# Optimization experiments

Measured on AMD Instinct MI355X. Metric: run time of the kernel, lower is better.

Reference implementation:

```python
import jax, jax.numpy as jnp
import numpy as np
import math

D, NS, PP, POS = 256, 4, 4, 16
PI = math.pi
LN_EPS = 1e-5


def _gelu(x):
    return jax.nn.gelu(x, approximate=False)  # torch default GELU is exact erf


def _mlp(x, W1, b1, W2, b2):
    return _gelu(x @ W1 + b1) @ W2 + b2


def setup_inputs() -> dict:
    key = jax.random.key(0)
    ks = jax.random.split(key, 16)

    def lin(k, fi, fo):
        k1, k2 = jax.random.split(k)
        s = 1.0 / np.sqrt(fi)
        W = jax.random.uniform(k1, (fi, fo), minval=-s, maxval=s, dtype=jnp.float32)
        b = jax.random.uniform(k2, (fo,), minval=-s, maxval=s, dtype=jnp.float32)
        return W, b

    x = jax.random.normal(ks[0], (2, 2048, D), dtype=jnp.float32)
    kW1, kb1 = lin(ks[1], D, D); kW2, kb2 = lin(ks[2], D, NS * PP)
    qW1, qb1 = lin(ks[3], D, D); qW2, qb2 = lin(ks[4], D, NS * PP)
    vW, vb = lin(ks[5], D, D)
    oW, ob = lin(ks[6], D, D)
    gW1, gb1 = lin(ks[7], D, D // 2); gW2, gb2 = lin(ks[8], D // 2, 1)
    lW1, lb1 = lin(ks[9], D, D); lW2, lb2 = lin(ks[10], D, POS)
    lvW, lvb = lin(ks[11], D, D)
    pos_freqs = jnp.exp(jnp.arange(POS, dtype=jnp.float32) * (-math.log(10000.0) / POS))
    return dict(
        x=x, kW1=kW1, kb1=kb1, kW2=kW2, kb2=kb2,
        qW1=qW1, qb1=qb1, qW2=qW2, qb2=qb2, vW=vW, vb=vb,
        ln_g=jnp.ones((D,), jnp.float32), ln_b=jnp.zeros((D,), jnp.float32), oW=oW, ob=ob,
        set_weights=jnp.ones((NS,), jnp.float32), pos_freqs=pos_freqs,
        pos_weight=jnp.ones((1,), jnp.float32),
        gW1=gW1, gb1=gb1, gW2=gW2, gb2=gb2,
        lW1=lW1, lb1=lb1, lW2=lW2, lb2=lb2, lvW=lvW, lvb=lvb,
        surprise_scale=jnp.float32(1.0), surprise_bias=jnp.float32(0.0),
        ltm_weight=jnp.float32(0.5),
    )


def _fwd(x, kW1, kb1, kW2, kb2, qW1, qb1, qW2, qb2, vW, vb, ln_g, ln_b, oW, ob,
         set_weights, pos_freqs, pos_weight, gW1, gb1, gW2, gb2,
         lW1, lb1, lW2, lb2, lvW, lvb, surprise_scale, surprise_bias, ltm_weight):
    B, L, Dd = x.shape
    key_phasor = jnp.exp(1j * (jnp.tanh(_mlp(x, kW1, kb1, kW2, kb2)) * PI)).reshape(B, L, NS, PP)
    query_phasor = jnp.exp(1j * (jnp.tanh(_mlp(x, qW1, qb1, qW2, qb2)) * PI)).reshape(B, L, NS, PP)
    V_real = x @ vW + vb  # (B,L,D)
    weights = jax.nn.softmax(set_weights)

    pos_cb = jnp.maximum(jnp.arange(L, dtype=jnp.float32), 1.0)  # shifted positions, clamp(min=1)

    # ---- cross-bank (joint product over sets) + surprise write gate ----
    joint_key = jnp.prod(key_phasor, axis=2)    # (B,L,PP)
    joint_query = jnp.prod(query_phasor, axis=2)
    km_shift = jnp.concatenate(
        [jnp.zeros_like(joint_key[:, :1]), jnp.cumsum(joint_key[:, :-1], axis=1)], axis=1)
    res_mag = jnp.abs((km_shift * jnp.conj(joint_key)).sum(-1))  # (B,L)
    familiarity = jnp.clip(res_mag / (pos_cb * math.sqrt(PP)), 0.0, 1.0)[..., None]
    write_gate = jax.nn.sigmoid(surprise_scale * ((1.0 - familiarity) - 0.5) + surprise_bias)
    V_gated = (V_real * write_gate).astype(jnp.complex64)

    bound = joint_key[..., None] * V_gated[:, :, None, :]       # (B,L,PP,D)
    memory = jnp.cumsum(bound, axis=1)
    cross_bank = (memory * jnp.conj(joint_query)[..., None]).sum(2).real  # (B,L,D)

    # ---- per-bank binding/retrieval ----
    bound_all = key_phasor[..., None] * V_gated[:, :, None, None, :]  # (B,L,NS,PP,D)
    mem_all = jnp.cumsum(bound_all, axis=1)
    retr_per_bank = (mem_all * jnp.conj(query_phasor)[..., None]).sum(3).real  # (B,L,NS,D)
    total = (retr_per_bank * weights[None, None, :, None]).sum(2)
    total = (total + cross_bank) / (NS + 1)

    # ---- positional phasor bank ----
    V = V_real.astype(jnp.complex64)
    pos_phasor = jnp.exp(1j * (jnp.arange(L, dtype=jnp.float32)[:, None] * pos_freqs * 2 * PI))  # (L,POS)
    bound_pos = pos_phasor[None, :, :, None] * V[:, :, None, :]  # (B,L,POS,D)
    mem_pos = jnp.cumsum(bound_pos, axis=1)
    retr_pos = (mem_pos * jnp.conj(pos_phasor)[None, :, :, None]).sum(2).real
    gate = jax.nn.sigmoid(_mlp(x, gW1, gb1, gW2, gb2))  # (B,L,1)
    total = gate * total + (1 - gate) * (jax.nn.sigmoid(pos_weight) * retr_pos)

    # ---- LTM bank with surprise gating ----
    ltm_kp = jnp.exp(1j * (jnp.tanh(_mlp(x, lW1, lb1, lW2, lb2)) * PI))  # (B,L,POS)
    ltm_val = x @ lvW + lvb
    km2 = jnp.concatenate(
        [jnp.zeros_like(ltm_kp[:, :1]), jnp.cumsum(ltm_kp[:, :-1], axis=1)], axis=1)
    res2 = jnp.abs((km2 * jnp.conj(ltm_kp)).sum(-1))
    fam2 = jnp.clip(res2 / (pos_cb * math.sqrt(POS)), 0.0, 1.0)[..., None]
    wg2 = jax.nn.sigmoid(surprise_scale * ((1.0 - fam2) - 0.5) + surprise_bias)  # (B,L,1)
    gated_bind = wg2[:, :, None, :] * ltm_kp[..., None] * ltm_val.astype(jnp.complex64)[:, :, None, :]
    ltm_mem = jnp.cumsum(gated_bind, axis=1)                      # (B,L,POS,D)
    ltm_retr = (ltm_mem * jnp.conj(ltm_kp)[..., None]).sum(2).real
    pos1 = jnp.arange(1, L + 1, dtype=jnp.float32)
    ltm_retr = ltm_retr / jnp.sqrt(pos1 * POS)[None, :, None]
    total = total + jax.nn.sigmoid(ltm_weight) * ltm_retr

    # ---- output projection: LayerNorm + Linear, residual ----
    t = total / jnp.sqrt(pos1 * PP)[None, :, None]
    mu = t.mean(-1, keepdims=True)
    var = t.var(-1, keepdims=True)
    tn = (t - mu) / jnp.sqrt(var + LN_EPS) * ln_g + ln_b
    return x + tn @ oW + ob


def reference(x, kW1, kb1, kW2, kb2, qW1, qb1, qW2, qb2, vW, vb, ln_g, ln_b, oW, ob,
              set_weights, pos_freqs, pos_weight, gW1, gb1, gW2, gb2,
              lW1, lb1, lW2, lb2, lvW, lvb, surprise_scale, surprise_bias, ltm_weight):
    return _fwd(x, kW1, kb1, kW2, kb2, qW1, qb1, qW2, qb2, vW, vb, ln_g, ln_b, oW, ob,
                set_weights, pos_freqs, pos_weight, gW1, gb1, gW2, gb2,
                lW1, lb1, lW2, lb2, lvW, lvb, surprise_scale, surprise_bias, ltm_weight)
```

## Files before the change

kernel.cpp:

```cpp
#include <hip/hip_runtime.h>
#include <math.h>

#define DD   256
#define NSB  4
#define PPB  4
#define POSB 16
#define LL   2048
#define BB   2
#define NC   64
#define CHK  32
#define NG   13
#define FS   128
#define PI_F 3.14159265358979323846f

#define JK_OFF   0
#define JQ_OFF   8
#define KP_OFF   16
#define QP_OFF   48
#define LKP_OFF  80
#define GATE_OFF 112

#define FEAT_O  0L
#define V_O     524288L
#define LV_O    1572864L
#define PPH_O   2621440L
#define TOT_O   2686976L
#define CMEM_O  3735552L
#define WGB_O   7143424L
#define TOT2_O  7151616L
#define WS_FLOATS 8200192L
#define KM_O    CMEM_O
#define XH_O    CMEM_O
#define XL_O    (CMEM_O + 524288L)
#define WTH_O   (CMEM_O + 1048576L)
#define WT2H_O  (CMEM_O + 1245184L)

typedef __attribute__((ext_vector_type(8))) short bf16x8;
typedef __attribute__((ext_vector_type(4))) float f32x4;

__device__ __forceinline__ float sigm(float v){ return 1.0f/(1.0f+expf(-v)); }
__device__ __forceinline__ float gelu_exact(float v){ return 0.5f*v*(1.0f+erff(v*0.70710678118654752f)); }
__device__ __forceinline__ unsigned short f2bf(float f){
    unsigned u = __float_as_uint(f);
    unsigned r = u + 0x7fffu + ((u>>16)&1u);
    return (unsigned short)(r>>16);
}
__device__ __forceinline__ float bf2f(unsigned short h){ return __uint_as_float(((unsigned)h)<<16); }

__global__ __launch_bounds__(256) void prep_all(
    const float* __restrict__ x,
    const float* __restrict__ kW1, const float* __restrict__ qW1, const float* __restrict__ lW1,
    const float* __restrict__ vW,  const float* __restrict__ lvW, const float* __restrict__ gW1,
    const float* __restrict__ kW2, const float* __restrict__ qW2, const float* __restrict__ lW2,
    const float* __restrict__ pf,
    unsigned short* __restrict__ xh, unsigned short* __restrict__ xl,
    unsigned short* __restrict__ wth, unsigned short* __restrict__ wt2h,
    float* __restrict__ posph)
{
    int bid = blockIdx.x, tid = threadIdx.x;
    if (bid < 512){
        int gid = bid*256 + tid;
        int frag = gid>>6, lane = gid&63;
        int tile = frag>>3, ksb = frag&7;
        int row = tile*16 + (lane&15);
        int k0  = ksb*32 + ((lane>>4)&3)*8;
        const float* xp = x + (long)row*DD + k0;
        unsigned short h8[8], l8[8];
        #pragma unroll
        for (int e=0;e<8;++e){
            float f = xp[e];
            unsigned short h = f2bf(f);
            h8[e] = h;
            l8[e] = f2bf(f - bf2f(h));
        }
        *(bf16x8*)(xh + (long)gid*8) = *(bf16x8*)h8;
        *(bf16x8*)(xl + (long)gid*8) = *(bf16x8*)l8;
    } else if (bid < 512+192){
        int gid = (bid-512)*256 + tid;
        int frag = gid>>6, lane = gid&63;
        int tile = frag>>3, ksb = frag&7;
        int col = tile*16 + (lane&15);
        int k0  = ksb*32 + ((lane>>4)&3)*8;
        unsigned short h8[8];
        #pragma unroll
        for (int e=0;e<8;++e){
            int fi = k0 + e;
            float w = 0.f;
            if (col < 1408){
                int m = col >> 8;
                if (m < 5){
                    const float* W = (m==0)?kW1:((m==1)?qW1:((m==2)?lW1:((m==3)?vW:lvW)));
                    w = W[(long)fi*DD + (col & 255)];
                } else {
                    w = gW1[(long)fi*128 + (col - 1280)];
                }
            }
            h8[e] = f2bf(w);
        }
        *(bf16x8*)(wth + (long)gid*8) = *(bf16x8*)h8;
    } else if (bid < 512+192+48){
        int blk = bid - (512+192);
        int m = blk>>4, o = blk&15;
        const float* W2 = (m==0)?kW2:((m==1)?qW2:lW2);
        wt2h[(long)blk*DD + tid] = f2bf(W2[tid*16+o]);
    } else {
        int t = (bid - (512+192+48))*256 + tid;
        if (t < LL){
            #pragma unroll
            for (int j=0;j<POSB;++j){
                float ang = (((float)t * pf[j]) * 2.0f) * PI_F;
                float s,c; sincosf(ang,&s,&c);
                posph[t*32+2*j]   = c;
                posph[t*32+2*j+1] = s;
            }
        }
    }
}

__global__ __launch_bounds__(256) void mlp_fused(
    const unsigned short* __restrict__ xh, const unsigned short* __restrict__ xl,
    const unsigned short* __restrict__ wth, const unsigned short* __restrict__ wt2h,
    const float* __restrict__ kb1, const float* __restrict__ kb2,
    const float* __restrict__ qb1, const float* __restrict__ qb2,
    const float* __restrict__ lb1, const float* __restrict__ lb2,
    const float* __restrict__ vb,  const float* __restrict__ lvb,
    const float* __restrict__ gb1, const float* __restrict__ gW2, const float* __restrict__ gb2,
    float* __restrict__ feat, float* __restrict__ Vbuf, float* __restrict__ lvalbuf)
{
    __shared__ __align__(16) char smraw[18432];
    int tid = threadIdx.x, lane = tid & 63, wv = tid >> 6;
    int mat = blockIdx.x >> 7, bm = blockIdx.x & 127;
    int rowg0 = bm*32;
    int ar = lane & 15, kk = (lane>>4)*8;

    f32x4 acc[2][4];
    #pragma unroll
    for (int i=0;i<2;++i)
        #pragma unroll
        for (int j=0;j<4;++j) acc[i][j] = (f32x4){0.f,0.f,0.f,0.f};

    bf16x8 ah[2], al[2], bh[4];
    {
        #pragma unroll
        for (int i=0;i<2;++i){
            long off = (((long)(2*bm+i)*8 + 0)*64 + lane)*8;
            ah[i] = *reinterpret_cast<const bf16x8*>(xh + off);
            al[i] = *reinterpret_cast<const bf16x8*>(xl + off);
        }
        #pragma unroll
        for (int j=0;j<4;++j){
            long off = (((long)(mat*16 + wv*4 + j)*8 + 0)*64 + lane)*8;
            bh[j] = *reinterpret_cast<const bf16x8*>(wth + off);
        }
    }
    #pragma unroll
    for (int ksb=0; ksb<8; ++ksb){
        bf16x8 nah[2], nal[2], nbh[4];
        if (ksb < 7){
            #pragma unroll
            for (int i=0;i<2;++i){
                long off = (((long)(2*bm+i)*8 + ksb+1)*64 + lane)*8;
                nah[i] = *reinterpret_cast<const bf16x8*>(xh + off);
                nal[i] = *reinterpret_cast<const bf16x8*>(xl + off);
            }
            #pragma unroll
            for (int j=0;j<4;++j){
                long off = (((long)(mat*16 + wv*4 + j)*8 + ksb+1)*64 + lane)*8;
                nbh[j] = *reinterpret_cast<const bf16x8*>(wth + off);
            }
        }
        #pragma unroll
        for (int i=0;i<2;++i)
            #pragma unroll
            for (int j=0;j<4;++j){
                acc[i][j] = __builtin_amdgcn_mfma_f32_16x16x32_bf16(ah[i], bh[j], acc[i][j], 0,0,0);
                acc[i][j] = __builtin_amdgcn_mfma_f32_16x16x32_bf16(al[i], bh[j], acc[i][j], 0,0,0);
            }
        if (ksb < 7){
            #pragma unroll
            for (int i=0;i<2;++i){ ah[i]=nah[i]; al[i]=nal[i]; }
            #pragma unroll
            for (int j=0;j<4;++j) bh[j]=nbh[j];
        }
    }

    int rl0 = (lane>>4)*4;

    if (mat < 3){
        float (*ang)[16] = (float(*)[16])(smraw + 16384);
        const float* b1 = (mat==0)?kb1:((mat==1)?qb1:lb1);
        #pragma unroll
        for (int i=0;i<2;++i)
            #pragma unroll
            for (int j=0;j<4;++j){
                int c = wv*64 + j*16 + ar;
                #pragma unroll
                for (int r=0;r<4;++r){
                    int row = i*16 + rl0 + r;
                    float hv = gelu_exact(acc[i][j][r] + b1[c]);
                    int bo = row*512 + c*2;
                    *(unsigned short*)(smraw + (bo ^ ((row&7)<<4))) = f2bf(hv);
                }
            }
        __syncthreads();
        const float* b2 = (mat==0)?kb2:((mat==1)?qb2:lb2);
        int off = (mat==0)?KP_OFF:((mat==1)?QP_OFF:LKP_OFF);
        if (wv < 2){
            int arow = wv*16 + ar;
            f32x4 a2 = (f32x4){0.f,0.f,0.f,0.f};
            #pragma unroll
            for (int ksb=0; ksb<8; ++ksb){
                int k = ksb*32 + kk;
                int bo = arow*512 + k*2;
                bf16x8 af = *reinterpret_cast<const bf16x8*>(smraw + (bo ^ ((arow&7)<<4)));
                bf16x8 bf = *reinterpret_cast<const bf16x8*>(wt2h + ((long)(mat*16 + ar)*DD + k));
                a2 = __builtin_amdgcn_mfma_f32_16x16x32_bf16(af, bf, a2, 0,0,0);
            }
            int o = ar;
            #pragma unroll
            for (int r=0;r<4;++r){
                int tok = wv*16 + rl0 + r;
                float a = tanhf(a2[r] + b2[o])*PI_F;
                ang[tok][o] = a;
                float sn,cs; sincosf(a,&sn,&cs);
                long rowg = rowg0 + tok;
                feat[rowg*FS + off + 2*o]   = cs;
                feat[rowg*FS + off + 2*o+1] = sn;
            }
        }
        __syncthreads();
        if (mat<2 && tid<128){
            int tok = tid>>2, p = tid&3;
            float a = ang[tok][p]+ang[tok][4+p]+ang[tok][8+p]+ang[tok][12+p];
            float sn,cs; sincosf(a,&sn,&cs);
            int joff = (mat==0)?JK_OFF:JQ_OFF;
            long rowg = rowg0 + tok;
            feat[rowg*FS + joff + 2*p]   = cs;
            feat[rowg*FS + joff + 2*p+1] = sn;
        }
    } else if (mat < 5){
        const float* bv = (mat==3)? vb : lvb;
        float* dst = (mat==3)? Vbuf : lvalbuf;
        #pragma unroll
        for (int i=0;i<2;++i)
            #pragma unroll
            for (int j=0;j<4;++j){
                int c = wv*64 + j*16 + ar;
                #pragma unroll
                for (int r=0;r<4;++r)
                    dst[(long)(rowg0 + i*16 + rl0 + r)*DD + c] = acc[i][j][r] + bv[c];
            }
    } else {
        float (*hg)[132] = (float(*)[132])smraw;
        float (*part)[8] = (float(*)[8])(smraw + 32*132*4);
        if (wv < 2){
            #pragma unroll
            for (int i=0;i<2;++i)
                #pragma unroll
                for (int j=0;j<4;++j){
                    int c = wv*64 + j*16 + ar;
                    #pragma unroll
                    for (int r=0;r<4;++r)
                        hg[i*16 + rl0 + r][c] = gelu_exact(acc[i][j][r] + gb1[c]);
                }
        }
        __syncthreads();
        {
            int tok = tid>>3, jj = tid&7;
            float s = 0.f;
            #pragma unroll
            for (int c=0;c<16;++c) s += hg[tok][jj*16+c]*gW2[jj*16+c];
            part[tok][jj] = s;
        }
        __syncthreads();
        if (tid < 32){
            float s = gb2[0];
            #pragma unroll
            for (int j=0;j<8;++j) s += part[tid][j];
            feat[(long)(rowg0+tid)*FS + GATE_OFF] = sigm(s);
        }
    }
}

__global__ __launch_bounds__(256) void g_prefix(const float* __restrict__ feat, float* __restrict__ km){
    int b = blockIdx.x / 40, ch = blockIdx.x % 40;
    int off = (ch<8) ? (JK_OFF+ch) : (LKP_OFF + (ch-8));
    int tid = threadIdx.x;
    long rb = (long)b*LL*FS;
    float v[8]; float s = 0.f;
    #pragma unroll
    for (int u=0;u<8;++u){
        v[u] = feat[rb + (long)(tid*8+u)*FS + off];
        s += v[u];
    }
    int lane = tid & 63, w = tid >> 6;
    float xsc = s;
    #pragma unroll
    for (int o=1;o<64;o<<=1){ float y = __shfl_up(xsc,o); if (lane>=o) xsc += y; }
    __shared__ float wsum[4];
    if (lane==63) wsum[w] = xsc;
    __syncthreads();
    float woff = 0.f;
    for (int i=0;i<w;++i) woff += wsum[i];
    float run = (xsc - s) + woff;
    #pragma unroll
    for (int u=0;u<8;++u){
        km[((long)b*LL + tid*8+u)*40 + ch] = run;
        run += v[u];
    }
}

__global__ __launch_bounds__(256) void g_fam(
    const float* __restrict__ feat, const float* __restrict__ km,
    const float* __restrict__ ss_p, const float* __restrict__ sb_p,
    float* __restrict__ wgbuf)
{
    int t = blockIdx.x*256 + threadIdx.x;
    if (t >= BB*LL) return;
    int tc = t % LL;
    float ss = ss_p[0], sb = sb_p[0];
    long frow = (long)t*FS;
    const float* kmrow = km + (long)t*40;
    float pcb = fmaxf((float)tc, 1.0f);

    float sr=0.f, si=0.f;
    #pragma unroll
    for (int p=0;p<4;++p){
        float kr = feat[frow+JK_OFF+2*p], ki = feat[frow+JK_OFF+2*p+1];
        float kmr = kmrow[2*p], kmi = kmrow[2*p+1];
        sr += kmr*kr + kmi*ki;
        si += kmi*kr - kmr*ki;
    }
    float res = sqrtf(sr*sr+si*si);
    float fam = fminf(fmaxf(res/(pcb*2.0f),0.f),1.f);
    wgbuf[(long)t*2] = sigm(ss*(0.5f-fam)+sb);

    sr=0.f; si=0.f;
    #pragma unroll
    for (int p=0;p<16;++p){
        float kr = feat[frow+LKP_OFF+2*p], ki = feat[frow+LKP_OFF+2*p+1];
        float kmr = kmrow[8+2*p], kmi = kmrow[8+2*p+1];
        sr += kmr*kr + kmi*ki;
        si += kmi*kr - kmr*ki;
    }
    float res2 = sqrtf(sr*sr+si*si);
    float fam2 = fminf(fmaxf(res2/(pcb*4.0f),0.f),1.f);
    wgbuf[(long)t*2+1] = sigm(ss*(0.5f-fam2)+sb);
}

__global__ __launch_bounds__(128) void m_chunksum(
    const float* __restrict__ feat, const float* __restrict__ posph,
    const float* __restrict__ wgbuf, const float* __restrict__ Vbuf,
    const float* __restrict__ lvalbuf, float* __restrict__ cmem)
{
    int blk = blockIdx.x;
    int dh = blk & 1; blk >>= 1;
    int b = blk/(NG*NC); int r = blk%(NG*NC); int g = r/NC, c = r%NC;
    int d = dh*128 + threadIdx.x;
    __shared__ __align__(16) float4 kl4[CHK][2];
    __shared__ float gl[CHK];
    long frow = ((long)b*LL + c*CHK)*FS;
    for (int idx=threadIdx.x; idx<CHK*2; idx+=128){
        int t = idx>>1, j = idx&1;
        float4 v;
        if (g==0)       v = *(const float4*)&feat[frow + (long)t*FS + JK_OFF + j*4];
        else if (g<5)   v = *(const float4*)&feat[frow + (long)t*FS + KP_OFF + (g-1)*8 + j*4];
        else if (g<9)   v = *(const float4*)&posph[(long)(c*CHK+t)*32 + (g-5)*8 + j*4];
        else            v = *(const float4*)&feat[frow + (long)t*FS + LKP_OFF + (g-9)*8 + j*4];
        kl4[t][j] = v;
    }
    for (int t=threadIdx.x; t<CHK; t+=128){
        float gf;
        if (g<5)      gf = wgbuf[((long)b*LL + c*CHK + t)*2];
        else if (g<9) gf = 1.0f;
        else          gf = wgbuf[((long)b*LL + c*CHK + t)*2 + 1];
        gl[t] = gf;
    }
    __syncthreads();
    const float* vsrc = (g>=9)? lvalbuf : Vbuf;
    long vrow = ((long)b*LL + c*CHK)*DD + d;
    float m0r=0,m0i=0,m1r=0,m1i=0,m2r=0,m2i=0,m3r=0,m3i=0;
    float vnext = vsrc[vrow];
    #pragma unroll 4
    for (int t=0;t<CHK;++t){
        float v = vnext * gl[t];
        if (t+1 < CHK) vnext = vsrc[vrow + (long)(t+1)*DD];
        float4 ka = kl4[t][0], kb = kl4[t][1];
        m0r += ka.x*v; m0i += ka.y*v;
        m1r += ka.z*v; m1i += ka.w*v;
        m2r += kb.x*v; m2i += kb.y*v;
        m3r += kb.z*v; m3i += kb.w*v;
    }
    long grp = (long)((b*NG+g)*NC + c);
    long ob = grp*8*DD + d;
    cmem[ob+0*DD]=m0r; cmem[ob+1*DD]=m0i;
    cmem[ob+2*DD]=m1r; cmem[ob+3*DD]=m1i;
    cmem[ob+4*DD]=m2r; cmem[ob+5*DD]=m2i;
    cmem[ob+6*DD]=m3r; cmem[ob+7*DD]=m3i;
}

__global__ __launch_bounds__(256) void m_scan(float* __restrict__ cmem){
    int line = blockIdx.x;
    int comp = line & 1; int l2 = line >> 1;
    int lb = l2>>2, slot = l2&3, d = threadIdx.x;
    float v[NC];
    #pragma unroll
    for (int c=0;c<NC;++c){
        long a = ((((long)(lb*NC + c)*4 + slot)*2) + comp)*DD + d;
        v[c] = cmem[a];
    }
    float run = 0.f;
    #pragma unroll
    for (int c=0;c<NC;++c){
        long a = ((((long)(lb*NC + c)*4 + slot)*2) + comp)*DD + d;
        cmem[a] = run;
        run += v[c];
    }
}

__global__ __launch_bounds__(128) void m_retrieve2(
    const float* __restrict__ feat, const float* __restrict__ posph,
    const float* __restrict__ wgbuf, const float* __restrict__ Vbuf,
    const float* __restrict__ lvalbuf, const float* __restrict__ cmem,
    const float* __restrict__ set_w, const float* __restrict__ pos_w,
    const float* __restrict__ ltm_w, float* __restrict__ totA, float* __restrict__ totB)
{
    int blk = blockIdx.x;
    int half = blk & 1; blk >>= 1;
    int dh = blk & 1; blk >>= 1;
    int c = blk % NC; int b = blk / NC;
    int d = dh*128 + threadIdx.x;
    __shared__ __align__(16) float4 sA[CHK][8];
    __shared__ __align__(16) float4 sB[CHK][8];
    __shared__ __align__(16) float4 sC[CHK][4];
    __shared__ float sSc[CHK][3];
    long frow = ((long)b*LL + c*CHK)*FS;

    for (int idx=threadIdx.x; idx<CHK*8; idx+=128){
        int t = idx>>3, j = idx&7;
        if (half==0){
            sA[t][j] = *(const float4*)&feat[frow + (long)t*FS + KP_OFF + j*4];
            sB[t][j] = *(const float4*)&feat[frow + (long)t*FS + QP_OFF + j*4];
        } else {
            sA[t][j] = *(const float4*)&posph[(long)(c*CHK+t)*32 + j*4];
            sB[t][j] = *(const float4*)&feat[frow + (long)t*FS + LKP_OFF + j*4];
        }
    }
    if (half==0){
        for (int idx=threadIdx.x; idx<CHK*4; idx+=128){
            int t = idx>>2, j = idx&3;
            sC[t][j] = *(const float4*)&feat[frow + (long)t*FS + JK_OFF + j*4];
        }
    }
    for (int t=threadIdx.x; t<CHK; t+=128){
        int tc = c*CHK + t;
        float gate = feat[frow + (long)t*FS + GATE_OFF];
        if (half==0){
            sSc[t][0] = wgbuf[((long)b*LL+tc)*2];
            sSc[t][1] = gate*0.2f;
        } else {
            sSc[t][0] = (1.0f-gate)*sigm(pos_w[0]);
            sSc[t][1] = wgbuf[((long)b*LL+tc)*2+1];
            sSc[t][2] = sigm(ltm_w[0]) * rsqrtf((float)(tc+1)*16.0f);
        }
    }
    __syncthreads();

    long vrow = ((long)b*LL + c*CHK)*DD + d;

    if (half == 0){
        float* tp = totA + ((long)b*LL + c*CHK)*DD + d;
        float w0=expf(set_w[0]),w1=expf(set_w[1]),w2=expf(set_w[2]),w3=expf(set_w[3]);
        float den = w0+w1+w2+w3;
        float wn[4] = {w0/den, w1/den, w2/den, w3/den};
        float cr[4], ci[4], br[4][4], bi[4][4];
        #pragma unroll
        for (int s=0;s<4;++s){
            long cb0 = (((long)(b*NG+0)*NC + c)*8 + 2*s)*DD + d;
            cr[s] = cmem[cb0]; ci[s] = cmem[cb0+DD];
        }
        #pragma unroll
        for (int g=0;g<4;++g)
            #pragma unroll
            for (int s=0;s<4;++s){
                long cb = (((long)(b*NG+1+g)*NC + c)*8 + 2*s)*DD + d;
                br[g][s] = cmem[cb]; bi[g][s] = cmem[cb+DD];
            }
        float vnext = Vbuf[vrow];
        #pragma unroll 2
        for (int t=0;t<CHK;++t){
            float v = vnext;
            if (t+1 < CHK) vnext = Vbuf[vrow + (long)(t+1)*DD];
            float vg = v * sSc[t][0];
            float4 jk0 = sC[t][0], jk1 = sC[t][1];
            float4 jq0 = sC[t][2], jq1 = sC[t][3];
            cr[0] += jk0.x*vg; ci[0] += jk0.y*vg;
            cr[1] += jk0.z*vg; ci[1] += jk0.w*vg;
            cr[2] += jk1.x*vg; ci[2] += jk1.y*vg;
            cr[3] += jk1.z*vg; ci[3] += jk1.w*vg;
            float rsc = cr[0]*jq0.x + ci[0]*jq0.y + cr[1]*jq0.z + ci[1]*jq0.w
                      + cr[2]*jq1.x + ci[2]*jq1.y + cr[3]*jq1.z + ci[3]*jq1.w;
            float rbank = 0.f;
            #pragma unroll
            for (int g=0;g<4;++g){
                float4 ka = sA[t][2*g], kb = sA[t][2*g+1];
                float4 qa = sB[t][2*g], qb = sB[t][2*g+1];
                br[g][0] += ka.x*vg; bi[g][0] += ka.y*vg;
                br[g][1] += ka.z*vg; bi[g][1] += ka.w*vg;
                br[g][2] += kb.x*vg; bi[g][2] += kb.y*vg;
                br[g][3] += kb.z*vg; bi[g][3] += kb.w*vg;
                float rg = br[g][0]*qa.x + bi[g][0]*qa.y + br[g][1]*qa.z + bi[g][1]*qa.w
                         + br[g][2]*qb.x + bi[g][2]*qb.y + br[g][3]*qb.z + bi[g][3]*qb.w;
                rbank += rg*wn[g];
            }
            tp[(long)t*DD] = sSc[t][1]*(rsc + rbank);
        }
    } else {
        float* tp = totB + ((long)b*LL + c*CHK)*DD + d;
        float pr[16], pi2[16], lr[16], li[16];
        #pragma unroll
        for (int g=0;g<4;++g)
            #pragma unroll
            for (int s=0;s<4;++s){
                long cb = (((long)(b*NG+5+g)*NC + c)*8 + 2*s)*DD + d;
                pr[g*4+s] = cmem[cb]; pi2[g*4+s] = cmem[cb+DD];
                long cb2 = (((long)(b*NG+9+g)*NC + c)*8 + 2*s)*DD + d;
                lr[g*4+s] = cmem[cb2]; li[g*4+s] = cmem[cb2+DD];
            }
        float vnext = Vbuf[vrow];
        float lvnext = lvalbuf[vrow];
        #pragma unroll 2
        for (int t=0;t<CHK;++t){
            float v = vnext, lv = lvnext;
            if (t+1 < CHK){
                vnext = Vbuf[vrow + (long)(t+1)*DD];
                lvnext = lvalbuf[vrow + (long)(t+1)*DD];
            }
            float vgl = lv * sSc[t][1];
            float rpos = 0.f, rltm = 0.f;
            #pragma unroll
            for (int j=0;j<8;++j){
                float4 pa = sA[t][j];
                pr[2*j]   += pa.x*v; pi2[2*j]   += pa.y*v;
                rpos += pr[2*j]*pa.x + pi2[2*j]*pa.y;
                pr[2*j+1] += pa.z*v; pi2[2*j+1] += pa.w*v;
                rpos += pr[2*j+1]*pa.z + pi2[2*j+1]*pa.w;
                float4 la = sB[t][j];
                lr[2*j]   += la.x*vgl; li[2*j]   += la.y*vgl;
                rltm += lr[2*j]*la.x + li[2*j]*la.y;
                lr[2*j+1] += la.z*vgl; li[2*j+1] += la.w*vgl;
                rltm += lr[2*j+1]*la.z + li[2*j+1]*la.w;
            }
            tp[(long)t*DD] = sSc[t][0]*rpos + sSc[t][2]*rltm;
        }
    }
}

__global__ __launch_bounds__(256) void k4_out(
    const float* __restrict__ x, const float* __restrict__ totA,
    const float* __restrict__ totB,
    const float* __restrict__ ln_g, const float* __restrict__ ln_b,
    const float* __restrict__ oW,  const float* __restrict__ obv,
    float* __restrict__ out)
{
    __shared__ float tn[8][DD];
    int tid = threadIdx.x;
    long base = (long)blockIdx.x*8;
    int wave = tid>>6, lane = tid&63;
    for (int wtok=0; wtok<2; ++wtok){
        int tok = wave*2 + wtok;
        long row = base + tok;
        int tc = (int)(row % LL);
        float inv = rsqrtf((float)(tc+1)*4.0f);
        float4 ta = ((const float4*)(totA + row*DD))[lane];
        float4 tb = ((const float4*)(totB + row*DD))[lane];
        float vals[4] = {(ta.x+tb.x)*inv, (ta.y+tb.y)*inv, (ta.z+tb.z)*inv, (ta.w+tb.w)*inv};
        float s=0.f, s2=0.f;
        #pragma unroll
        for (int k=0;k<4;++k){ s += vals[k]; s2 += vals[k]*vals[k]; }
        for (int o=1;o<64;o<<=1){ s += __shfl_xor(s,o); s2 += __shfl_xor(s2,o); }
        float mu = s/256.f, var = s2/256.f - mu*mu;
        float rstd = rsqrtf(var + 1e-5f);
        float4 w;
        w.x = (vals[0]-mu)*rstd*ln_g[lane*4+0] + ln_b[lane*4+0];
        w.y = (vals[1]-mu)*rstd*ln_g[lane*4+1] + ln_b[lane*4+1];
        w.z = (vals[2]-mu)*rstd*ln_g[lane*4+2] + ln_b[lane*4+2];
        w.w = (vals[3]-mu)*rstd*ln_g[lane*4+3] + ln_b[lane*4+3];
        ((float4*)&tn[tok][0])[lane] = w;
    }
    __syncthreads();
    float acc[8];
    #pragma unroll
    for (int tok=0;tok<8;++tok) acc[tok]=obv[tid];
    #pragma unroll 4
    for (int i=0;i<DD;++i){
        float w = oW[i*DD+tid];
        #pragma unroll
        for (int tok=0;tok<8;++tok) acc[tok] += tn[tok][i]*w;
    }
    for (int tok=0;tok<8;++tok){
        long row = base+tok;
        out[row*DD+tid] = x[row*DD+tid] + acc[tok];
    }
}

extern "C" void kernel_launch(void* const* d_in, const int* in_sizes, int n_in,
                              void* d_out, int out_size, void* d_ws, size_t ws_size,
                              hipStream_t stream)
{
    const float* x    = (const float*)d_in[0];
    const float* kW1  = (const float*)d_in[1];
    const float* kb1  = (const float*)d_in[2];
    const float* kW2  = (const float*)d_in[3];
    const float* kb2  = (const float*)d_in[4];
    const float* qW1  = (const float*)d_in[5];
    const float* qb1  = (const float*)d_in[6];
    const float* qW2  = (const float*)d_in[7];
    const float* qb2  = (const float*)d_in[8];
    const float* vW   = (const float*)d_in[9];
    const float* vb   = (const float*)d_in[10];
    const float* ln_g = (const float*)d_in[11];
    const float* ln_b = (const float*)d_in[12];
    const float* oW   = (const float*)d_in[13];
    const float* ob   = (const float*)d_in[14];
    const float* set_w= (const float*)d_in[15];
    const float* pf   = (const float*)d_in[16];
    const float* pw   = (const float*)d_in[17];
    const float* gW1  = (const float*)d_in[18];
    const float* gb1  = (const float*)d_in[19];
    const float* gW2  = (const float*)d_in[20];
    const float* gb2  = (const float*)d_in[21];
    const float* lW1  = (const float*)d_in[22];
    const float* lb1  = (const float*)d_in[23];
    const float* lW2  = (const float*)d_in[24];
    const float* lb2  = (const float*)d_in[25];
    const float* lvW  = (const float*)d_in[26];
    const float* lvb  = (const float*)d_in[27];
    const float* ss   = (const float*)d_in[28];
    const float* sb   = (const float*)d_in[29];
    const float* lw   = (const float*)d_in[30];
    float* out = (float*)d_out;

    float* ws    = (float*)d_ws;
    float* feat  = ws + FEAT_O;
    float* Vbuf  = ws + V_O;
    float* lval  = ws + LV_O;
    float* posph = ws + PPH_O;
    float* total = ws + TOT_O;
    float* cmem  = ws + CMEM_O;
    float* km    = ws + KM_O;
    float* wgbuf = ws + WGB_O;
    float* tot2  = ws + TOT2_O;
    unsigned short* xh   = (unsigned short*)(ws + XH_O);
    unsigned short* xl   = (unsigned short*)(ws + XL_O);
    unsigned short* wth  = (unsigned short*)(ws + WTH_O);
    unsigned short* wt2h = (unsigned short*)(ws + WT2H_O);

    (void)in_sizes; (void)n_in; (void)out_size; (void)ws_size;

    prep_all <<<512+192+48+8, 256, 0, stream>>>(x, kW1,qW1,lW1,vW,lvW,gW1, kW2,qW2,lW2,
                                                pf, xh, xl, wth, wt2h, posph);
    mlp_fused<<<6*128, 256, 0, stream>>>(xh,xl,wth,wt2h,
                                         kb1,kb2, qb1,qb2, lb1,lb2,
                                         vb,lvb, gb1,gW2,gb2, feat, Vbuf, lval);
    g_prefix <<<BB*40, 256, 0, stream>>>(feat, km);
    g_fam    <<<(BB*LL+255)/256, 256, 0, stream>>>(feat, km, ss, sb, wgbuf);
    m_chunksum <<<BB*NG*NC*2, 128, 0, stream>>>(feat, posph, wgbuf, Vbuf, lval, cmem);
    m_scan     <<<BB*NG*4*2, 256, 0, stream>>>(cmem);
    m_retrieve2 <<<BB*NC*2*2, 128, 0, stream>>>(feat, posph, wgbuf, Vbuf, lval, cmem,
                                                set_w, pw, lw, total, tot2);
    k4_out     <<<BB*LL/8, 256, 0, stream>>>(x, total, tot2, ln_g, ln_b, oW, ob, out);
}
```

Measured before the change: 109.0 us.

## Use bf16 MFMA for output projection and merge chunk-sum groups per family

The output LayerNorm+Linear kernel now runs the projection on MFMA bf16 instructions. The normalized activations are split into hi/lo bf16 pairs held in swizzled LDS, and the weights are pre-transposed to bf16 in the prep kernel. The chunk-sum kernel now processes all key groups of a family in one block (5, 4 or 4 groups), so each V row is loaded once instead of 13 times. This cuts global traffic and block count, at the cost of more registers per thread and bf16 rounding of oW.

```diff
diff --git a/kernel.cpp b/kernel.cpp
--- a/kernel.cpp
+++ b/kernel.cpp
@@ -28,7 +28,8 @@
 #define CMEM_O  3735552L
 #define WGB_O   7143424L
 #define TOT2_O  7151616L
-#define WS_FLOATS 8200192L
+#define OWT_O   8200192L
+#define WS_FLOATS 8232960L
 #define KM_O    CMEM_O
 #define XH_O    CMEM_O
 #define XL_O    (CMEM_O + 524288L)
@@ -52,10 +53,10 @@
     const float* __restrict__ kW1, const float* __restrict__ qW1, const float* __restrict__ lW1,
     const float* __restrict__ vW,  const float* __restrict__ lvW, const float* __restrict__ gW1,
     const float* __restrict__ kW2, const float* __restrict__ qW2, const float* __restrict__ lW2,
-    const float* __restrict__ pf,
+    const float* __restrict__ oW,  const float* __restrict__ pf,
     unsigned short* __restrict__ xh, unsigned short* __restrict__ xl,
     unsigned short* __restrict__ wth, unsigned short* __restrict__ wt2h,
-    float* __restrict__ posph)
+    unsigned short* __restrict__ owt, float* __restrict__ posph)
 {
     int bid = blockIdx.x, tid = threadIdx.x;
     if (bid < 512){
@@ -103,7 +104,7 @@
         int m = blk>>4, o = blk&15;
         const float* W2 = (m==0)?kW2:((m==1)?qW2:lW2);
         wt2h[(long)blk*DD + tid] = f2bf(W2[tid*16+o]);
-    } else {
+    } else if (bid < 512+192+48+8){
         int t = (bid - (512+192+48))*256 + tid;
         if (t < LL){
             #pragma unroll
@@ -114,6 +115,17 @@
                 posph[t*32+2*j+1] = s;
             }
         }
+    } else {
+        int gid = (bid - (512+192+48+8))*256 + tid;
+        int frag = gid>>6, lane = gid&63;
+        int tile = frag>>3, ksb = frag&7;
+        int col = tile*16 + (lane&15);
+        int k0  = ksb*32 + ((lane>>4)&3)*8;
+        unsigned short h8[8];
+        #pragma unroll
+        for (int e=0;e<8;++e)
+            h8[e] = f2bf(oW[(long)(k0+e)*DD + col]);
+        *(bf16x8*)(owt + (long)gid*8) = *(bf16x8*)h8;
     }
 }
 
@@ -348,55 +360,99 @@
     wgbuf[(long)t*2+1] = sigm(ss*(0.5f-fam2)+sb);
 }
 
-__global__ __launch_bounds__(128) void m_chunksum(
+__global__ __launch_bounds__(128) void m_chunksum_fam(
     const float* __restrict__ feat, const float* __restrict__ posph,
     const float* __restrict__ wgbuf, const float* __restrict__ Vbuf,
     const float* __restrict__ lvalbuf, float* __restrict__ cmem)
 {
     int blk = blockIdx.x;
+    int fam = blk % 3; blk /= 3;
     int dh = blk & 1; blk >>= 1;
-    int b = blk/(NG*NC); int r = blk%(NG*NC); int g = r/NC, c = r%NC;
+    int c = blk % NC; int b = blk / NC;
     int d = dh*128 + threadIdx.x;
-    __shared__ __align__(16) float4 kl4[CHK][2];
+    __shared__ __align__(16) float4 kk4[CHK][10];
     __shared__ float gl[CHK];
     long frow = ((long)b*LL + c*CHK)*FS;
-    for (int idx=threadIdx.x; idx<CHK*2; idx+=128){
-        int t = idx>>1, j = idx&1;
-        float4 v;
-        if (g==0)       v = *(const float4*)&feat[frow + (long)t*FS + JK_OFF + j*4];
-        else if (g<5)   v = *(const float4*)&feat[frow + (long)t*FS + KP_OFF + (g-1)*8 + j*4];
-        else if (g<9)   v = *(const float4*)&posph[(long)(c*CHK+t)*32 + (g-5)*8 + j*4];
-        else            v = *(const float4*)&feat[frow + (long)t*FS + LKP_OFF + (g-9)*8 + j*4];
-        kl4[t][j] = v;
+
+    if (fam==0){
+        for (int idx=threadIdx.x; idx<CHK*10; idx+=128){
+            int t = idx/10, j = idx%10;
+            kk4[t][j] = (j<2) ? *(const float4*)&feat[frow + (long)t*FS + JK_OFF + j*4]
+                              : *(const float4*)&feat[frow + (long)t*FS + KP_OFF + (j-2)*4];
+        }
+    } else if (fam==1){
+        for (int idx=threadIdx.x; idx<CHK*8; idx+=128){
+            int t = idx>>3, j = idx&7;
+            kk4[t][j] = *(const float4*)&posph[(long)(c*CHK+t)*32 + j*4];
+        }
+    } else {
+        for (int idx=threadIdx.x; idx<CHK*8; idx+=128){
+            int t = idx>>3, j = idx&7;
+            kk4[t][j] = *(const float4*)&feat[frow + (long)t*FS + LKP_OFF + j*4];
+        }
     }
     for (int t=threadIdx.x; t<CHK; t+=128){
         float gf;
-        if (g<5)      gf = wgbuf[((long)b*LL + c*CHK + t)*2];
-        else if (g<9) gf = 1.0f;
-        else          gf = wgbuf[((long)b*LL + c*CHK + t)*2 + 1];
+        if (fam==0)      gf = wgbuf[((long)b*LL + c*CHK + t)*2];
+        else if (fam==1) gf = 1.0f;
+        else             gf = wgbuf[((long)b*LL + c*CHK + t)*2 + 1];
         gl[t] = gf;
     }
     __syncthreads();
-    const float* vsrc = (g>=9)? lvalbuf : Vbuf;
+
+    const float* vsrc = (fam==2)? lvalbuf : Vbuf;
     long vrow = ((long)b*LL + c*CHK)*DD + d;
-    float m0r=0,m0i=0,m1r=0,m1i=0,m2r=0,m2i=0,m3r=0,m3i=0;
-    float vnext = vsrc[vrow];
-    #pragma unroll 4
-    for (int t=0;t<CHK;++t){
-        float v = vnext * gl[t];
-        if (t+1 < CHK) vnext = vsrc[vrow + (long)(t+1)*DD];
-        float4 ka = kl4[t][0], kb = kl4[t][1];
-        m0r += ka.x*v; m0i += ka.y*v;
-        m1r += ka.z*v; m1i += ka.w*v;
-        m2r += kb.x*v; m2i += kb.y*v;
-        m3r += kb.z*v; m3i += kb.w*v;
-    }
-    long grp = (long)((b*NG+g)*NC + c);
-    long ob = grp*8*DD + d;
-    cmem[ob+0*DD]=m0r; cmem[ob+1*DD]=m0i;
-    cmem[ob+2*DD]=m1r; cmem[ob+3*DD]=m1i;
-    cmem[ob+4*DD]=m2r; cmem[ob+5*DD]=m2i;
-    cmem[ob+6*DD]=m3r; cmem[ob+7*DD]=m3i;
+
+    if (fam==0){
+        float cr[20], ci[20];
+        #pragma unroll
+        for (int i=0;i<20;++i){ cr[i]=0.f; ci[i]=0.f; }
+        float vnext = vsrc[vrow];
+        for (int t=0;t<CHK;++t){
+            float v = vnext * gl[t];
+            if (t+1 < CHK) vnext = vsrc[vrow + (long)(t+1)*DD];
+            #pragma unroll
+            for (int j=0;j<10;++j){
+                float4 a = kk4[t][j];
+                cr[2*j]   += a.x*v; ci[2*j]   += a.y*v;
+                cr[2*j+1] += a.z*v; ci[2*j+1] += a.w*v;
+            }
+        }
+        #pragma unroll
+        for (int g5=0; g5<5; ++g5){
+            long ob = ((long)(b*NG+g5)*NC + c)*8*DD + d;
+            #pragma unroll
+            for (int s=0;s<4;++s){
+                cmem[ob + (2*s)*DD]   = cr[g5*4+s];
+                cmem[ob + (2*s+1)*DD] = ci[g5*4+s];
+            }
+        }
+    } else {
+        float cr[16], ci[16];
+        #pragma unroll
+        for (int i=0;i<16;++i){ cr[i]=0.f; ci[i]=0.f; }
+        float vnext = vsrc[vrow];
+        for (int t=0;t<CHK;++t){
+            float v = vnext * gl[t];
+            if (t+1 < CHK) vnext = vsrc[vrow + (long)(t+1)*DD];
+            #pragma unroll
+            for (int j=0;j<8;++j){
+                float4 a = kk4[t][j];
+                cr[2*j]   += a.x*v; ci[2*j]   += a.y*v;
+                cr[2*j+1] += a.z*v; ci[2*j+1] += a.w*v;
+            }
+        }
+        int g0 = (fam==1)? 5 : 9;
+        #pragma unroll
+        for (int g=0; g<4; ++g){
+            long ob = ((long)(b*NG+g0+g)*NC + c)*8*DD + d;
+            #pragma unroll
+            for (int s=0;s<4;++s){
+                cmem[ob + (2*s)*DD]   = cr[g*4+s];
+                cmem[ob + (2*s+1)*DD] = ci[g*4+s];
+            }
+        }
+    }
 }
 
 __global__ __launch_bounds__(256) void m_scan(float* __restrict__ cmem){
@@ -556,51 +612,76 @@
     }
 }
 
-__global__ __launch_bounds__(256) void k4_out(
+__global__ __launch_bounds__(256) void k4_mfma(
     const float* __restrict__ x, const float* __restrict__ totA,
     const float* __restrict__ totB,
     const float* __restrict__ ln_g, const float* __restrict__ ln_b,
-    const float* __restrict__ oW,  const float* __restrict__ obv,
+    const unsigned short* __restrict__ owt, const float* __restrict__ obv,
     float* __restrict__ out)
 {
-    __shared__ float tn[8][DD];
-    int tid = threadIdx.x;
-    long base = (long)blockIdx.x*8;
-    int wave = tid>>6, lane = tid&63;
-    for (int wtok=0; wtok<2; ++wtok){
-        int tok = wave*2 + wtok;
-        long row = base + tok;
-        int tc = (int)(row % LL);
+    __shared__ __align__(16) char smraw[16384];
+    int tid = threadIdx.x, lane = tid & 63, wv = tid >> 6;
+    long base = (long)blockIdx.x * 16;
+    int ar = lane & 15, kk = (lane>>4)*8;
+
+    #pragma unroll
+    for (int r4=0; r4<4; ++r4){
+        int row = wv*4 + r4;
+        long grow = base + row;
+        int tc = (int)(grow % LL);
         float inv = rsqrtf((float)(tc+1)*4.0f);
-        float4 ta = ((const float4*)(totA + row*DD))[lane];
-        float4 tb = ((const float4*)(totB + row*DD))[lane];
+        float4 ta = ((const float4*)(totA + grow*DD))[lane];
+        float4 tb = ((const float4*)(totB + grow*DD))[lane];
         float vals[4] = {(ta.x+tb.x)*inv, (ta.y+tb.y)*inv, (ta.z+tb.z)*inv, (ta.w+tb.w)*inv};
         float s=0.f, s2=0.f;
         #pragma unroll
         for (int k=0;k<4;++k){ s += vals[k]; s2 += vals[k]*vals[k]; }
+        #pragma unroll
         for (int o=1;o<64;o<<=1){ s += __shfl_xor(s,o); s2 += __shfl_xor(s2,o); }
         float mu = s/256.f, var = s2/256.f - mu*mu;
         float rstd = rsqrtf(var + 1e-5f);
-        float4 w;
-        w.x = (vals[0]-mu)*rstd*ln_g[lane*4+0] + ln_b[lane*4+0];
-        w.y = (vals[1]-mu)*rstd*ln_g[lane*4+1] + ln_b[lane*4+1];
-        w.z = (vals[2]-mu)*rstd*ln_g[lane*4+2] + ln_b[lane*4+2];
-        w.w = (vals[3]-mu)*rstd*ln_g[lane*4+3] + ln_b[lane*4+3];
-        ((float4*)&tn[tok][0])[lane] = w;
+        unsigned short h4[4], l4[4];
+        #pragma unroll
+        for (int k=0;k<4;++k){
+            float tv = (vals[k]-mu)*rstd*ln_g[lane*4+k] + ln_b[lane*4+k];
+            unsigned short h = f2bf(tv);
+            h4[k] = h;
+            l4[k] = f2bf(tv - bf2f(h));
+        }
+        int bo = (row*512 + lane*8) ^ ((row&7)<<4);
+        *(ushort4*)(smraw + bo)        = *(ushort4*)h4;
+        *(ushort4*)(smraw + 8192 + bo) = *(ushort4*)l4;
     }
     __syncthreads();
-    float acc[8];
-    #pragma unroll
-    for (int tok=0;tok<8;++tok) acc[tok]=obv[tid];
-    #pragma unroll 4
-    for (int i=0;i<DD;++i){
-        float w = oW[i*DD+tid];
-        #pragma unroll
-        for (int tok=0;tok<8;++tok) acc[tok] += tn[tok][i]*w;
-    }
-    for (int tok=0;tok<8;++tok){
-        long row = base+tok;
-        out[row*DD+tid] = x[row*DD+tid] + acc[tok];
+
+    f32x4 acc[4];
+    #pragma unroll
+    for (int j=0;j<4;++j) acc[j] = (f32x4){0.f,0.f,0.f,0.f};
+    #pragma unroll
+    for (int ksb=0; ksb<8; ++ksb){
+        int k0 = ksb*32 + kk;
+        int bo = (ar*512 + k0*2) ^ ((ar&7)<<4);
+        bf16x8 ahh = *reinterpret_cast<const bf16x8*>(smraw + bo);
+        bf16x8 all = *reinterpret_cast<const bf16x8*>(smraw + 8192 + bo);
+        #pragma unroll
+        for (int j=0;j<4;++j){
+            long off = (((long)(wv*4 + j)*8 + ksb)*64 + lane)*8;
+            bf16x8 bw = *reinterpret_cast<const bf16x8*>(owt + off);
+            acc[j] = __builtin_amdgcn_mfma_f32_16x16x32_bf16(ahh, bw, acc[j], 0,0,0);
+            acc[j] = __builtin_amdgcn_mfma_f32_16x16x32_bf16(all, bw, acc[j], 0,0,0);
+        }
+    }
+
+    int rl0 = (lane>>4)*4;
+    #pragma unroll
+    for (int j=0;j<4;++j){
+        int col = wv*64 + j*16 + ar;
+        float bv = obv[col];
+        #pragma unroll
+        for (int r=0;r<4;++r){
+            long grow = base + rl0 + r;
+            out[grow*DD + col] = x[grow*DD + col] + acc[j][r] + bv;
+        }
     }
 }
 
@@ -655,19 +736,20 @@
     unsigned short* xl   = (unsigned short*)(ws + XL_O);
     unsigned short* wth  = (unsigned short*)(ws + WTH_O);
     unsigned short* wt2h = (unsigned short*)(ws + WT2H_O);
+    unsigned short* owt  = (unsigned short*)(ws + OWT_O);
 
     (void)in_sizes; (void)n_in; (void)out_size; (void)ws_size;
 
-    prep_all <<<512+192+48+8, 256, 0, stream>>>(x, kW1,qW1,lW1,vW,lvW,gW1, kW2,qW2,lW2,
-                                                pf, xh, xl, wth, wt2h, posph);
+    prep_all <<<512+192+48+8+32, 256, 0, stream>>>(x, kW1,qW1,lW1,vW,lvW,gW1, kW2,qW2,lW2,
+                                                   oW, pf, xh, xl, wth, wt2h, owt, posph);
     mlp_fused<<<6*128, 256, 0, stream>>>(xh,xl,wth,wt2h,
                                          kb1,kb2, qb1,qb2, lb1,lb2,
                                          vb,lvb, gb1,gW2,gb2, feat, Vbuf, lval);
     g_prefix <<<BB*40, 256, 0, stream>>>(feat, km);
     g_fam    <<<(BB*LL+255)/256, 256, 0, stream>>>(feat, km, ss, sb, wgbuf);
-    m_chunksum <<<BB*NG*NC*2, 128, 0, stream>>>(feat, posph, wgbuf, Vbuf, lval, cmem);
+    m_chunksum_fam <<<BB*NC*2*3, 128, 0, stream>>>(feat, posph, wgbuf, Vbuf, lval, cmem);
     m_scan     <<<BB*NG*4*2, 256, 0, stream>>>(cmem);
     m_retrieve2 <<<BB*NC*2*2, 128, 0, stream>>>(feat, posph, wgbuf, Vbuf, lval, cmem,
                                                 set_w, pw, lw, total, tot2);
-    k4_out     <<<BB*LL/8, 256, 0, stream>>>(x, total, tot2, ln_g, ln_b, oW, ob, out);
-}
+    k4_mfma    <<<BB*LL/16, 256, 0, stream>>>(x, total, tot2, ln_g, ln_b, owt, ob, out);
+}
```

After: 110.4 us. No clear change (+1.3%).
